# Kernel tuning notes

Hardware: AMD Instinct MI355X
Metric: run time of the kernel (lower is better)

## Reference

```python
import jax, jax.numpy as jnp
import numpy as np

B, DIN, H, DOUT, NB = 1024, 512, 1024, 512, 10
ALPHA = 0.5
INNER = 5


def setup_inputs() -> dict:
    key = jax.random.key(0)
    ks = jax.random.split(key, 5)
    return {
        "x": jax.random.normal(ks[0], (B, DIN), jnp.float32),
        "embed_W": jax.random.normal(ks[1], (H, DIN), jnp.float32) / np.float32(np.sqrt(DIN)),
        "embed_b": jnp.zeros((H,), jnp.float32),
        "block_W": jax.random.normal(ks[2], (NB, H, H), jnp.float32) * np.float32(0.8 / np.sqrt(H)),
        "block_b": jnp.zeros((NB, H), jnp.float32),
        "head_W": jax.random.normal(ks[3], (DOUT, H), jnp.float32) / np.float32(np.sqrt(H)),
        "head_b": jnp.zeros((DOUT,), jnp.float32),
        "steps": 30,
    }


def reference(x, embed_W, embed_b, block_W, block_b, head_W, head_b, steps):
    nb = block_W.shape[0]
    x_emb = x @ embed_W.T + embed_b  # [B, H]
    bb = block_b[:, None, :]  # [NB, 1, H]

    def inner_core(inp):
        # inp: [NB, B, H]; run inner equilibrium loop from h=0
        def body(h, _):
            pre = jnp.einsum('nbh,ndh->nbd', h, block_W) + bb + inp
            h = (1.0 - ALPHA) * h + ALPHA * jnp.tanh(pre)
            return h, None
        h, _ = jax.lax.scan(body, jnp.zeros_like(inp), None, length=INNER)
        return h

    def outer_step(h, _):
        # block i's input is previous-step state of block i-1 (block 0 gets x_emb)
        block_in = jnp.concatenate([x_emb[None], h[:-1]], axis=0)  # [NB, B, H]
        inner_eq = inner_core(h + block_in)
        h_new = (1.0 - ALPHA) * h + ALPHA * inner_eq
        return h_new, None

    h0 = jnp.zeros((nb,) + x_emb.shape, x_emb.dtype)
    h_final, _ = jax.lax.scan(outer_step, h0, None, length=steps)
    return h_final[-1] @ head_W.T + head_b  # [B, DOUT]
```

## Files before the change

kernel.cpp:

```cpp
#include <hip/hip_runtime.h>
#include <cstdint>
#include <cstddef>

#define B_DIM  1024
#define DIN    512
#define H_DIM  1024
#define DOUT   512
#define NB     10
#define STEPS  30

typedef _Float16 half_t;
typedef __attribute__((ext_vector_type(8))) _Float16 frag_ab;
typedef __attribute__((ext_vector_type(8))) _Float16 h8vec;
typedef __attribute__((ext_vector_type(4))) float    frag_cd;

__device__ __forceinline__ void gload16(const void* g, void* l) {
    __builtin_amdgcn_global_load_lds(
        (const __attribute__((address_space(1))) void*)g,
        (__attribute__((address_space(3))) void*)l, 16, 0, 0);
}

__device__ __forceinline__ float fast_tanh(float x) {
    float e, r;
    asm("v_exp_f32 %0, %1" : "=v"(e) : "v"(x * 2.8853900817779268f));
    asm("v_rcp_f32 %0, %1" : "=v"(r) : "v"(e + 1.0f));
    return __builtin_fmaf(-2.0f, r, 1.0f);
}

__global__ void __launch_bounds__(256)
f2h_kernel(const float* __restrict__ src, half_t* __restrict__ dst, int n4)
{
    const int i = blockIdx.x * 256 + threadIdx.x;
    if (i < n4) {
        const float4 v = ((const float4*)src)[i];
        half_t o[4] = { (half_t)v.x, (half_t)v.y, (half_t)v.z, (half_t)v.w };
        ((uint2*)dst)[i] = *(const uint2*)o;
    }
}

template <int MODE>
__global__ void __launch_bounds__(256, 2)
gemm_bt(const half_t* __restrict__ A,
        const half_t* __restrict__ W,
        const float* __restrict__ bias,
        const half_t* __restrict__ binp,
        const half_t* aux16,
        float* __restrict__ out32,
        half_t* out16,
        int M, int N, int K)
{
    const int gx  = gridDim.x, gy = gridDim.y;
    const int nwg = gx * gy * gridDim.z;
    const int f   = blockIdx.x + gx * (blockIdx.y + gy * blockIdx.z);
    const int w   = (f & 7) * (nwg >> 3) + (f >> 3);
    const int bx  = w % gx;
    const int rst = w / gx;
    const int by  = rst % gy;
    const int n   = rst / gy;

    A    += (size_t)n * M * K;
    W    += (size_t)n * N * K;
    bias += (size_t)n * N;
    if (MODE != 0) {
        const size_t so = (size_t)n * M * N;
        binp  += so;
        out16 += so;
        if (MODE == 2) aux16 += so;
    }

    const int tileM = by * 128;
    const int tileN = bx * 128;

    __shared__ __attribute__((aligned(16))) char lds_raw[65536];
    half_t* lA  = (half_t*)lds_raw;
    half_t* lB  = (half_t*)(lds_raw + 32768);
    float*  fsm = (float*)lds_raw;

    const int tid  = threadIdx.x;
    const int wave = tid >> 6;
    const int lane = tid & 63;
    const int q    = lane >> 4;
    const int r16  = lane & 15;
    const int wm   = wave >> 1;
    const int wn   = wave & 1;

    const int srow = lane >> 3;
    const int scol = ((lane & 7) ^ srow) * 8;

    const half_t* gA = A + (size_t)(tileM + wave * 32 + srow) * K + scol;
    const half_t* gW = W + (size_t)(tileN + wave * 32 + srow) * K + scol;

    auto stage = [&](int k0, int b) {
#pragma unroll
        for (int i = 0; i < 4; ++i)
            gload16(gA + (size_t)i * 8 * K + k0,
                    (void*)&lA[b * 8192 + (wave * 32 + i * 8) * 64]);
#pragma unroll
        for (int i = 0; i < 4; ++i)
            gload16(gW + (size_t)i * 8 * K + k0,
                    (void*)&lB[b * 8192 + (wave * 32 + i * 8) * 64]);
    };

    frag_cd acc[4][4];
#pragma unroll
    for (int mt = 0; mt < 4; ++mt)
#pragma unroll
        for (int nt = 0; nt < 4; ++nt)
            acc[mt][nt] = (frag_cd){0.f, 0.f, 0.f, 0.f};

    const int NT = K >> 6;
    stage(0, 0);

    int cur = 0;
    for (int t = 0; t < NT; ++t) {
        if (t + 1 < NT) {
            stage((t + 1) << 6, cur ^ 1);
            asm volatile("s_waitcnt vmcnt(8)" ::: "memory");
        } else {
            asm volatile("s_waitcnt vmcnt(0)" ::: "memory");
        }
        __builtin_amdgcn_s_barrier();
        asm volatile("" ::: "memory");

        frag_ab av[2][4], bv[2][4];
#pragma unroll
        for (int kk = 0; kk < 2; ++kk) {
            const int cb = ((kk * 4 + q) ^ (r16 & 7)) * 8;
#pragma unroll
            for (int mt = 0; mt < 4; ++mt)
                av[kk][mt] = *(const frag_ab*)&lA[cur * 8192 + (wm * 64 + mt * 16 + r16) * 64 + cb];
#pragma unroll
            for (int nt = 0; nt < 4; ++nt)
                bv[kk][nt] = *(const frag_ab*)&lB[cur * 8192 + (wn * 64 + nt * 16 + r16) * 64 + cb];
        }
#pragma unroll
        for (int kk = 0; kk < 2; ++kk)
#pragma unroll
            for (int mt = 0; mt < 4; ++mt)
#pragma unroll
                for (int nt = 0; nt < 4; ++nt)
                    acc[mt][nt] = __builtin_amdgcn_mfma_f32_16x16x32_f16(
                        av[kk][mt], bv[kk][nt], acc[mt][nt], 0, 0, 0);

        asm volatile("" ::: "memory");
        __builtin_amdgcn_s_barrier();
        cur ^= 1;
    }

    if (MODE == 0) {
#pragma unroll
        for (int mt = 0; mt < 4; ++mt)
#pragma unroll
            for (int nt = 0; nt < 4; ++nt)
#pragma unroll
                for (int r = 0; r < 4; ++r) {
                    const int row = tileM + wm * 64 + mt * 16 + q * 4 + r;
                    const int col = tileN + wn * 64 + nt * 16 + r16;
                    out32[(size_t)row * N + col] = acc[mt][nt][r] + bias[col];
                }
        return;
    }

#pragma unroll
    for (int mt = 0; mt < 4; ++mt)
#pragma unroll
        for (int nt = 0; nt < 4; ++nt)
#pragma unroll
            for (int r = 0; r < 4; ++r)
                fsm[(wm * 64 + mt * 16 + q * 4 + r) * 128 + wn * 64 + nt * 16 + r16]
                    = acc[mt][nt][r];
    __syncthreads();

#pragma unroll
    for (int c = 0; c < 8; ++c) {
        const int e   = (c * 256 + tid) * 8;
        const int rl  = e >> 7;
        const int cl  = e & 127;
        const int row = tileM + rl;
        const int col = tileN + cl;
        const size_t g = (size_t)row * N + col;

        const h8vec bi8 = *(const h8vec*)&binp[g];
        h8vec ho8, ax8;
        if (MODE == 1 || MODE == 2) ho8 = *(const h8vec*)&A[(size_t)row * K + col];
        if (MODE == 2)              ax8 = *(const h8vec*)&aux16[g];

        half_t o[8];
#pragma unroll
        for (int j = 0; j < 8; ++j) {
            const float v  = fsm[rl * 128 + cl + j];
            const float bi = (float)bi8[j];
            const float tt = fast_tanh(v + bi);
            const float ho = (MODE == 3) ? 0.5f * fast_tanh(bi) : (float)ho8[j];
            const float hn = 0.5f * ho + 0.5f * tt;
            const float ov = (MODE == 2) ? 0.5f * (float)ax8[j] + 0.5f * hn : hn;
            o[j] = (half_t)ov;
        }
        *(uint4*)&out16[g] = *(const uint4*)o;
    }
}

__global__ void __launch_bounds__(256)
pre_outer_kernel(const half_t* __restrict__ h,
                 const float* __restrict__ x_emb,
                 const float* __restrict__ bb,
                 half_t* __restrict__ binp,
                 half_t* __restrict__ hhh)
{
    const int f  = blockIdx.x;
    const int k  = f & 7;
    const int j  = f >> 3;
    const int p  = 10 * k + (j % 10);
    const int bi = j / 10;
    const int n  = p >> 3;

    const size_t idx = ((size_t)p << 17) + (size_t)bi * 2048 + (size_t)threadIdx.x * 8;
    const size_t off = idx - (size_t)n * B_DIM * H_DIM;
    const int    col = (int)(off & (H_DIM - 1));

    const h8vec ha = *(const h8vec*)&h[idx];
    float pv[8];
    if (n == 0) {
        const float4 p0 = *(const float4*)&x_emb[off];
        const float4 p1 = *(const float4*)&x_emb[off + 4];
        pv[0] = p0.x; pv[1] = p0.y; pv[2] = p0.z; pv[3] = p0.w;
        pv[4] = p1.x; pv[5] = p1.y; pv[6] = p1.z; pv[7] = p1.w;
    } else {
        const h8vec pa = *(const h8vec*)&h[idx - (size_t)B_DIM * H_DIM];
#pragma unroll
        for (int j2 = 0; j2 < 8; ++j2) pv[j2] = (float)pa[j2];
    }
    const float4 b0 = *(const float4*)&bb[(size_t)n * H_DIM + col];
    const float4 b1 = *(const float4*)&bb[(size_t)n * H_DIM + col + 4];
    const float bp[8] = {b0.x, b0.y, b0.z, b0.w, b1.x, b1.y, b1.z, b1.w};

    half_t bv[8], hv[8];
#pragma unroll
    for (int j2 = 0; j2 < 8; ++j2) {
        const float biv = (float)ha[j2] + pv[j2] + bp[j2];
        bv[j2] = (half_t)biv;
        hv[j2] = (half_t)(0.5f * fast_tanh(biv));
    }
    *(uint4*)&binp[idx] = *(const uint4*)bv;
    *(uint4*)&hhh[idx]  = *(const uint4*)hv;
}

static inline void conv(const float* src, half_t* dst, int n, hipStream_t s) {
    const int n4 = n / 4;
    f2h_kernel<<<(n4 + 255) / 256, 256, 0, s>>>(src, dst, n4);
}

extern "C" void kernel_launch(void* const* d_in, const int* in_sizes, int n_in,
                              void* d_out, int out_size, void* d_ws, size_t ws_size,
                              hipStream_t stream)
{
    const float* x     = (const float*)d_in[0];
    const float* embW  = (const float*)d_in[1];
    const float* embB  = (const float*)d_in[2];
    const float* blkW  = (const float*)d_in[3];
    const float* blkB  = (const float*)d_in[4];
    const float* headW = (const float*)d_in[5];
    const float* headB = (const float*)d_in[6];
    float* out = (float*)d_out;

    char* ws = (char*)d_ws;
    size_t off = 0;
    auto alloc = [&](size_t bytes) {
        void* p = ws + off;
        off += (bytes + 255) & ~(size_t)255;
        return p;
    };
    const size_t NE = (size_t)NB * B_DIM * H_DIM;

    float* xemb32 = (float*)alloc((size_t)B_DIM * H_DIM * 4);
    half_t* h16    = (half_t*)alloc(NE * 2);
    half_t* binp16 = (half_t*)alloc(NE * 2);
    half_t* hhh0   = (half_t*)alloc(NE * 2);
    half_t* hhh1   = (half_t*)alloc(NE * 2);
    half_t* wx     = (half_t*)alloc((size_t)B_DIM * DIN * 2);
    half_t* wembW  = (half_t*)alloc((size_t)H_DIM * DIN * 2);
    half_t* wblkW  = (half_t*)alloc((size_t)NB * H_DIM * H_DIM * 2);
    half_t* wheadW = (half_t*)alloc((size_t)DOUT * H_DIM * 2);
    (void)ws_size;

    conv(x,     wx,     B_DIM * DIN,        stream);
    conv(embW,  wembW,  H_DIM * DIN,        stream);
    conv(blkW,  wblkW,  NB * H_DIM * H_DIM, stream);
    conv(headW, wheadW, DOUT * H_DIM,       stream);

    hipMemsetAsync(h16, 0, NE * 2, stream);

    const dim3 blk(256);

    gemm_bt<0><<<dim3(H_DIM / 128, B_DIM / 128, 1), blk, 0, stream>>>(
        wx, wembW, embB, nullptr, nullptr, xemb32, nullptr, B_DIM, H_DIM, DIN);

    const dim3 ggrid(H_DIM / 128, B_DIM / 128, NB);
    const int pre_blocks = (int)(NE / (8 * 256));
    for (int s = 0; s < STEPS; ++s) {
        pre_outer_kernel<<<pre_blocks, blk, 0, stream>>>(h16, xemb32, blkB, binp16, hhh0);
        gemm_bt<3><<<ggrid, blk, 0, stream>>>(hhh0, wblkW, blkB, binp16, nullptr,
                                              nullptr, hhh1, B_DIM, H_DIM, H_DIM);
        gemm_bt<1><<<ggrid, blk, 0, stream>>>(hhh1, wblkW, blkB, binp16, nullptr,
                                              nullptr, hhh0, B_DIM, H_DIM, H_DIM);
        gemm_bt<1><<<ggrid, blk, 0, stream>>>(hhh0, wblkW, blkB, binp16, nullptr,
                                              nullptr, hhh1, B_DIM, H_DIM, H_DIM);
        gemm_bt<2><<<ggrid, blk, 0, stream>>>(hhh1, wblkW, blkB, binp16, h16,
                                              nullptr, h16, B_DIM, H_DIM, H_DIM);
    }

    gemm_bt<0><<<dim3(DOUT / 128, B_DIM / 128, 1), blk, 0, stream>>>(
        h16 + (size_t)(NB - 1) * B_DIM * H_DIM, wheadW, headB, nullptr, nullptr,
        out, nullptr, B_DIM, DOUT, H_DIM);
}
```

Before: 4.594 ms.

## Halve GEMM K-tile and LDS footprint to fit four workgroups per CU

```diff
diff --git a/kernel.cpp b/kernel.cpp
--- a/kernel.cpp
+++ b/kernel.cpp
@@ -39,7 +39,7 @@
 }
 
 template <int MODE>
-__global__ void __launch_bounds__(256, 2)
+__global__ void __launch_bounds__(256, 4)
 gemm_bt(const half_t* __restrict__ A,
         const half_t* __restrict__ W,
         const float* __restrict__ bias,
@@ -71,9 +71,9 @@
     const int tileM = by * 128;
     const int tileN = bx * 128;
 
-    __shared__ __attribute__((aligned(16))) char lds_raw[65536];
+    __shared__ __attribute__((aligned(16))) char lds_raw[32768];
     half_t* lA  = (half_t*)lds_raw;
-    half_t* lB  = (half_t*)(lds_raw + 32768);
+    half_t* lB  = (half_t*)(lds_raw + 16384);
     float*  fsm = (float*)lds_raw;
 
     const int tid  = threadIdx.x;
@@ -84,21 +84,20 @@
     const int wm   = wave >> 1;
     const int wn   = wave & 1;
 
-    const int srow = lane >> 3;
-    const int scol = ((lane & 7) ^ srow) * 8;
+    const int srow = lane >> 2;
+    const int scol = ((lane & 3) ^ ((srow >> 1) & 3)) * 8;
 
     const half_t* gA = A + (size_t)(tileM + wave * 32 + srow) * K + scol;
     const half_t* gW = W + (size_t)(tileN + wave * 32 + srow) * K + scol;
 
     auto stage = [&](int k0, int b) {
 #pragma unroll
-        for (int i = 0; i < 4; ++i)
-            gload16(gA + (size_t)i * 8 * K + k0,
-                    (void*)&lA[b * 8192 + (wave * 32 + i * 8) * 64]);
-#pragma unroll
-        for (int i = 0; i < 4; ++i)
-            gload16(gW + (size_t)i * 8 * K + k0,
-                    (void*)&lB[b * 8192 + (wave * 32 + i * 8) * 64]);
+        for (int i = 0; i < 2; ++i) {
+            gload16(gA + (size_t)i * 16 * K + k0,
+                    (void*)&lA[b * 4096 + (wave * 32 + i * 16) * 32]);
+            gload16(gW + (size_t)i * 16 * K + k0,
+                    (void*)&lB[b * 4096 + (wave * 32 + i * 16) * 32]);
+        }
     };
 
     frag_cd acc[4][4];
@@ -108,39 +107,35 @@
         for (int nt = 0; nt < 4; ++nt)
             acc[mt][nt] = (frag_cd){0.f, 0.f, 0.f, 0.f};
 
-    const int NT = K >> 6;
+    const int NT = K >> 5;
     stage(0, 0);
+
+    const int cb = (q ^ ((r16 >> 1) & 3)) * 8;
 
     int cur = 0;
     for (int t = 0; t < NT; ++t) {
         if (t + 1 < NT) {
-            stage((t + 1) << 6, cur ^ 1);
-            asm volatile("s_waitcnt vmcnt(8)" ::: "memory");
+            stage((t + 1) << 5, cur ^ 1);
+            asm volatile("s_waitcnt vmcnt(4)" ::: "memory");
         } else {
             asm volatile("s_waitcnt vmcnt(0)" ::: "memory");
         }
         __builtin_amdgcn_s_barrier();
         asm volatile("" ::: "memory");
 
-        frag_ab av[2][4], bv[2][4];
-#pragma unroll
-        for (int kk = 0; kk < 2; ++kk) {
-            const int cb = ((kk * 4 + q) ^ (r16 & 7)) * 8;
-#pragma unroll
-            for (int mt = 0; mt < 4; ++mt)
-                av[kk][mt] = *(const frag_ab*)&lA[cur * 8192 + (wm * 64 + mt * 16 + r16) * 64 + cb];
+        frag_ab av[4], bv[4];
+#pragma unroll
+        for (int mt = 0; mt < 4; ++mt)
+            av[mt] = *(const frag_ab*)&lA[cur * 4096 + (wm * 64 + mt * 16 + r16) * 32 + cb];
+#pragma unroll
+        for (int nt = 0; nt < 4; ++nt)
+            bv[nt] = *(const frag_ab*)&lB[cur * 4096 + (wn * 64 + nt * 16 + r16) * 32 + cb];
+#pragma unroll
+        for (int mt = 0; mt < 4; ++mt)
 #pragma unroll
             for (int nt = 0; nt < 4; ++nt)
-                bv[kk][nt] = *(const frag_ab*)&lB[cur * 8192 + (wn * 64 + nt * 16 + r16) * 64 + cb];
-        }
-#pragma unroll
-        for (int kk = 0; kk < 2; ++kk)
-#pragma unroll
-            for (int mt = 0; mt < 4; ++mt)
-#pragma unroll
-                for (int nt = 0; nt < 4; ++nt)
-                    acc[mt][nt] = __builtin_amdgcn_mfma_f32_16x16x32_f16(
-                        av[kk][mt], bv[kk][nt], acc[mt][nt], 0, 0, 0);
+                acc[mt][nt] = __builtin_amdgcn_mfma_f32_16x16x32_f16(
+                    av[mt], bv[nt], acc[mt][nt], 0, 0, 0);
 
         asm volatile("" ::: "memory");
         __builtin_amdgcn_s_barrier();
@@ -161,42 +156,58 @@
         return;
     }
 
-#pragma unroll
-    for (int mt = 0; mt < 4; ++mt)
-#pragma unroll
-        for (int nt = 0; nt < 4; ++nt)
-#pragma unroll
-            for (int r = 0; r < 4; ++r)
-                fsm[(wm * 64 + mt * 16 + q * 4 + r) * 128 + wn * 64 + nt * 16 + r16]
-                    = acc[mt][nt][r];
-    __syncthreads();
-
-#pragma unroll
-    for (int c = 0; c < 8; ++c) {
-        const int e   = (c * 256 + tid) * 8;
-        const int rl  = e >> 7;
-        const int cl  = e & 127;
-        const int row = tileM + rl;
-        const int col = tileN + cl;
-        const size_t g = (size_t)row * N + col;
-
-        const h8vec bi8 = *(const h8vec*)&binp[g];
-        h8vec ho8, ax8;
-        if (MODE == 1 || MODE == 2) ho8 = *(const h8vec*)&A[(size_t)row * K + col];
-        if (MODE == 2)              ax8 = *(const h8vec*)&aux16[g];
-
-        half_t o[8];
-#pragma unroll
-        for (int j = 0; j < 8; ++j) {
-            const float v  = fsm[rl * 128 + cl + j];
-            const float bi = (float)bi8[j];
-            const float tt = fast_tanh(v + bi);
-            const float ho = (MODE == 3) ? 0.5f * fast_tanh(bi) : (float)ho8[j];
-            const float hn = 0.5f * ho + 0.5f * tt;
-            const float ov = (MODE == 2) ? 0.5f * (float)ax8[j] + 0.5f * hn : hn;
-            o[j] = (half_t)ov;
+    for (int pass = 0; pass < 2; ++pass) {
+        __syncthreads();
+        if (wm == pass) {
+#pragma unroll
+            for (int mt = 0; mt < 4; ++mt)
+#pragma unroll
+                for (int nt = 0; nt < 4; ++nt)
+#pragma unroll
+                    for (int r = 0; r < 4; ++r) {
+                        const int rowl = mt * 16 + q * 4 + r;
+                        const int col  = wn * 64 + nt * 16 + r16;
+                        const int g    = col >> 2;
+                        const int gl   = (g & 24) | ((g ^ (g >> 3) ^ (rowl & 7)) & 7);
+                        fsm[rowl * 128 + gl * 4 + (col & 3)] = acc[mt][nt][r];
+                    }
         }
-        *(uint4*)&out16[g] = *(const uint4*)o;
+        __syncthreads();
+
+#pragma unroll
+        for (int c = 0; c < 4; ++c) {
+            const int e    = (c * 256 + tid) * 8;
+            const int rowl = e >> 7;
+            const int col0 = e & 127;
+            const int row  = tileM + pass * 64 + rowl;
+            const int col  = tileN + col0;
+            const size_t gidx = (size_t)row * N + col;
+
+            const int g0  = col0 >> 2;
+            const int gl0 = (g0 & 24) | ((g0 ^ (g0 >> 3) ^ (rowl & 7)) & 7);
+            const int g1  = g0 + 1;
+            const int gl1 = (g1 & 24) | ((g1 ^ (g1 >> 3) ^ (rowl & 7)) & 7);
+            const float4 va = *(const float4*)&fsm[rowl * 128 + gl0 * 4];
+            const float4 vb = *(const float4*)&fsm[rowl * 128 + gl1 * 4];
+            const float vv[8] = {va.x, va.y, va.z, va.w, vb.x, vb.y, vb.z, vb.w};
+
+            const h8vec bi8 = *(const h8vec*)&binp[gidx];
+            h8vec ho8, ax8;
+            if (MODE == 1 || MODE == 2) ho8 = *(const h8vec*)&A[(size_t)row * K + col];
+            if (MODE == 2)              ax8 = *(const h8vec*)&aux16[gidx];
+
+            half_t o[8];
+#pragma unroll
+            for (int j = 0; j < 8; ++j) {
+                const float bi = (float)bi8[j];
+                const float tt = fast_tanh(vv[j] + bi);
+                const float ho = (MODE == 3) ? 0.5f * fast_tanh(bi) : (float)ho8[j];
+                const float hn = 0.5f * ho + 0.5f * tt;
+                const float ov = (MODE == 2) ? 0.5f * (float)ax8[j] + 0.5f * hn : hn;
+                o[j] = (half_t)ov;
+            }
+            *(uint4*)&out16[gidx] = *(const uint4*)o;
+        }
     }
 }
 
```

Result: slower. 6.757 ms (+47.1%).

## Use persistent 512-block grid with per-XCD tile assignment and swizzled epilogue LDS

Applied to the files above, without the earlier changes.

```diff
diff --git a/kernel.cpp b/kernel.cpp
--- a/kernel.cpp
+++ b/kernel.cpp
@@ -49,28 +49,6 @@
         half_t* out16,
         int M, int N, int K)
 {
-    const int gx  = gridDim.x, gy = gridDim.y;
-    const int nwg = gx * gy * gridDim.z;
-    const int f   = blockIdx.x + gx * (blockIdx.y + gy * blockIdx.z);
-    const int w   = (f & 7) * (nwg >> 3) + (f >> 3);
-    const int bx  = w % gx;
-    const int rst = w / gx;
-    const int by  = rst % gy;
-    const int n   = rst / gy;
-
-    A    += (size_t)n * M * K;
-    W    += (size_t)n * N * K;
-    bias += (size_t)n * N;
-    if (MODE != 0) {
-        const size_t so = (size_t)n * M * N;
-        binp  += so;
-        out16 += so;
-        if (MODE == 2) aux16 += so;
-    }
-
-    const int tileM = by * 128;
-    const int tileN = bx * 128;
-
     __shared__ __attribute__((aligned(16))) char lds_raw[65536];
     half_t* lA  = (half_t*)lds_raw;
     half_t* lB  = (half_t*)(lds_raw + 32768);
@@ -87,116 +65,165 @@
     const int srow = lane >> 3;
     const int scol = ((lane & 7) ^ srow) * 8;
 
-    const half_t* gA = A + (size_t)(tileM + wave * 32 + srow) * K + scol;
-    const half_t* gW = W + (size_t)(tileN + wave * 32 + srow) * K + scol;
-
-    auto stage = [&](int k0, int b) {
-#pragma unroll
-        for (int i = 0; i < 4; ++i)
-            gload16(gA + (size_t)i * 8 * K + k0,
-                    (void*)&lA[b * 8192 + (wave * 32 + i * 8) * 64]);
-#pragma unroll
-        for (int i = 0; i < 4; ++i)
-            gload16(gW + (size_t)i * 8 * K + k0,
-                    (void*)&lB[b * 8192 + (wave * 32 + i * 8) * 64]);
+    auto do_tile = [&](int bx, int by, int n) {
+        const half_t* An = A + (size_t)n * M * K;
+        const half_t* Wn = W + (size_t)n * N * K;
+        const float*  bn = bias + (size_t)n * N;
+        const half_t* binpn = binp;
+        const half_t* auxn  = aux16;
+        half_t* outn = out16;
+        if (MODE != 0) {
+            const size_t so = (size_t)n * M * N;
+            binpn = binp + so;
+            outn  = out16 + so;
+            if (MODE == 2) auxn = aux16 + so;
+        }
+        const int tileM = by * 128;
+        const int tileN = bx * 128;
+
+        const half_t* gA = An + (size_t)(tileM + wave * 32 + srow) * K + scol;
+        const half_t* gW = Wn + (size_t)(tileN + wave * 32 + srow) * K + scol;
+
+        auto stage = [&](int k0, int b) {
+#pragma unroll
+            for (int i = 0; i < 4; ++i)
+                gload16(gA + (size_t)i * 8 * K + k0,
+                        (void*)&lA[b * 8192 + (wave * 32 + i * 8) * 64]);
+#pragma unroll
+            for (int i = 0; i < 4; ++i)
+                gload16(gW + (size_t)i * 8 * K + k0,
+                        (void*)&lB[b * 8192 + (wave * 32 + i * 8) * 64]);
+        };
+
+        frag_cd acc[4][4];
+#pragma unroll
+        for (int mt = 0; mt < 4; ++mt)
+#pragma unroll
+            for (int nt = 0; nt < 4; ++nt)
+                acc[mt][nt] = (frag_cd){0.f, 0.f, 0.f, 0.f};
+
+        __syncthreads();
+        const int NT = K >> 6;
+        stage(0, 0);
+
+        int cur = 0;
+        for (int t = 0; t < NT; ++t) {
+            if (t + 1 < NT) {
+                stage((t + 1) << 6, cur ^ 1);
+                asm volatile("s_waitcnt vmcnt(8)" ::: "memory");
+            } else {
+                asm volatile("s_waitcnt vmcnt(0)" ::: "memory");
+            }
+            __builtin_amdgcn_s_barrier();
+            asm volatile("" ::: "memory");
+
+            frag_ab av[2][4], bv[2][4];
+#pragma unroll
+            for (int kk = 0; kk < 2; ++kk) {
+                const int cb = ((kk * 4 + q) ^ (r16 & 7)) * 8;
+#pragma unroll
+                for (int mt = 0; mt < 4; ++mt)
+                    av[kk][mt] = *(const frag_ab*)&lA[cur * 8192 + (wm * 64 + mt * 16 + r16) * 64 + cb];
+#pragma unroll
+                for (int nt = 0; nt < 4; ++nt)
+                    bv[kk][nt] = *(const frag_ab*)&lB[cur * 8192 + (wn * 64 + nt * 16 + r16) * 64 + cb];
+            }
+#pragma unroll
+            for (int kk = 0; kk < 2; ++kk)
+#pragma unroll
+                for (int mt = 0; mt < 4; ++mt)
+#pragma unroll
+                    for (int nt = 0; nt < 4; ++nt)
+                        acc[mt][nt] = __builtin_amdgcn_mfma_f32_16x16x32_f16(
+                            av[kk][mt], bv[kk][nt], acc[mt][nt], 0, 0, 0);
+
+            asm volatile("" ::: "memory");
+            __builtin_amdgcn_s_barrier();
+            cur ^= 1;
+        }
+
+        if (MODE == 0) {
+#pragma unroll
+            for (int mt = 0; mt < 4; ++mt)
+#pragma unroll
+                for (int nt = 0; nt < 4; ++nt)
+#pragma unroll
+                    for (int r = 0; r < 4; ++r) {
+                        const int row = tileM + wm * 64 + mt * 16 + q * 4 + r;
+                        const int col = tileN + wn * 64 + nt * 16 + r16;
+                        out32[(size_t)row * N + col] = acc[mt][nt][r] + bn[col];
+                    }
+            return;
+        }
+
+#pragma unroll
+        for (int mt = 0; mt < 4; ++mt)
+#pragma unroll
+            for (int nt = 0; nt < 4; ++nt)
+#pragma unroll
+                for (int r = 0; r < 4; ++r) {
+                    const int row = wm * 64 + mt * 16 + q * 4 + r;
+                    const int col = wn * 64 + nt * 16 + r16;
+                    const int g   = col >> 2;
+                    const int gl  = (g & 24) | ((g ^ (g >> 3) ^ (row & 7)) & 7);
+                    fsm[row * 128 + gl * 4 + (col & 3)] = acc[mt][nt][r];
+                }
+        __syncthreads();
+
+#pragma unroll
+        for (int c = 0; c < 8; ++c) {
+            const int e   = (c * 256 + tid) * 8;
+            const int rl  = e >> 7;
+            const int cl  = e & 127;
+            const int row = tileM + rl;
+            const int col = tileN + cl;
+            const size_t gidx = (size_t)row * N + col;
+
+            const int g0  = cl >> 2;
+            const int gl0 = (g0 & 24) | ((g0 ^ (g0 >> 3) ^ (rl & 7)) & 7);
+            const int g1  = g0 + 1;
+            const int gl1 = (g1 & 24) | ((g1 ^ (g1 >> 3) ^ (rl & 7)) & 7);
+            const float4 va = *(const float4*)&fsm[rl * 128 + gl0 * 4];
+            const float4 vb = *(const float4*)&fsm[rl * 128 + gl1 * 4];
+            const float vv[8] = {va.x, va.y, va.z, va.w, vb.x, vb.y, vb.z, vb.w};
+
+            const h8vec bi8 = *(const h8vec*)&binpn[gidx];
+            h8vec ho8, ax8;
+            if (MODE == 1 || MODE == 2) ho8 = *(const h8vec*)&An[(size_t)row * K + col];
+            if (MODE == 2)              ax8 = *(const h8vec*)&auxn[gidx];
+
+            half_t o[8];
+#pragma unroll
+            for (int j = 0; j < 8; ++j) {
+                const float bi = (float)bi8[j];
+                const float tt = fast_tanh(vv[j] + bi);
+                const float ho = (MODE == 3) ? 0.5f * fast_tanh(bi) : (float)ho8[j];
+                const float hn = 0.5f * ho + 0.5f * tt;
+                const float ov = (MODE == 2) ? 0.5f * (float)ax8[j] + 0.5f * hn : hn;
+                o[j] = (half_t)ov;
+            }
+            *(uint4*)&outn[gidx] = *(const uint4*)o;
+        }
     };
 
-    frag_cd acc[4][4];
-#pragma unroll
-    for (int mt = 0; mt < 4; ++mt)
-#pragma unroll
-        for (int nt = 0; nt < 4; ++nt)
-            acc[mt][nt] = (frag_cd){0.f, 0.f, 0.f, 0.f};
-
-    const int NT = K >> 6;
-    stage(0, 0);
-
-    int cur = 0;
-    for (int t = 0; t < NT; ++t) {
-        if (t + 1 < NT) {
-            stage((t + 1) << 6, cur ^ 1);
-            asm volatile("s_waitcnt vmcnt(8)" ::: "memory");
-        } else {
-            asm volatile("s_waitcnt vmcnt(0)" ::: "memory");
-        }
-        __builtin_amdgcn_s_barrier();
-        asm volatile("" ::: "memory");
-
-        frag_ab av[2][4], bv[2][4];
-#pragma unroll
-        for (int kk = 0; kk < 2; ++kk) {
-            const int cb = ((kk * 4 + q) ^ (r16 & 7)) * 8;
-#pragma unroll
-            for (int mt = 0; mt < 4; ++mt)
-                av[kk][mt] = *(const frag_ab*)&lA[cur * 8192 + (wm * 64 + mt * 16 + r16) * 64 + cb];
-#pragma unroll
-            for (int nt = 0; nt < 4; ++nt)
-                bv[kk][nt] = *(const frag_ab*)&lB[cur * 8192 + (wn * 64 + nt * 16 + r16) * 64 + cb];
-        }
-#pragma unroll
-        for (int kk = 0; kk < 2; ++kk)
-#pragma unroll
-            for (int mt = 0; mt < 4; ++mt)
-#pragma unroll
-                for (int nt = 0; nt < 4; ++nt)
-                    acc[mt][nt] = __builtin_amdgcn_mfma_f32_16x16x32_f16(
-                        av[kk][mt], bv[kk][nt], acc[mt][nt], 0, 0, 0);
-
-        asm volatile("" ::: "memory");
-        __builtin_amdgcn_s_barrier();
-        cur ^= 1;
-    }
-
     if (MODE == 0) {
-#pragma unroll
-        for (int mt = 0; mt < 4; ++mt)
-#pragma unroll
-            for (int nt = 0; nt < 4; ++nt)
-#pragma unroll
-                for (int r = 0; r < 4; ++r) {
-                    const int row = tileM + wm * 64 + mt * 16 + q * 4 + r;
-                    const int col = tileN + wn * 64 + nt * 16 + r16;
-                    out32[(size_t)row * N + col] = acc[mt][nt][r] + bias[col];
-                }
-        return;
-    }
-
-#pragma unroll
-    for (int mt = 0; mt < 4; ++mt)
-#pragma unroll
-        for (int nt = 0; nt < 4; ++nt)
-#pragma unroll
-            for (int r = 0; r < 4; ++r)
-                fsm[(wm * 64 + mt * 16 + q * 4 + r) * 128 + wn * 64 + nt * 16 + r16]
-                    = acc[mt][nt][r];
-    __syncthreads();
-
-#pragma unroll
-    for (int c = 0; c < 8; ++c) {
-        const int e   = (c * 256 + tid) * 8;
-        const int rl  = e >> 7;
-        const int cl  = e & 127;
-        const int row = tileM + rl;
-        const int col = tileN + cl;
-        const size_t g = (size_t)row * N + col;
-
-        const h8vec bi8 = *(const h8vec*)&binp[g];
-        h8vec ho8, ax8;
-        if (MODE == 1 || MODE == 2) ho8 = *(const h8vec*)&A[(size_t)row * K + col];
-        if (MODE == 2)              ax8 = *(const h8vec*)&aux16[g];
-
-        half_t o[8];
-#pragma unroll
-        for (int j = 0; j < 8; ++j) {
-            const float v  = fsm[rl * 128 + cl + j];
-            const float bi = (float)bi8[j];
-            const float tt = fast_tanh(v + bi);
-            const float ho = (MODE == 3) ? 0.5f * fast_tanh(bi) : (float)ho8[j];
-            const float hn = 0.5f * ho + 0.5f * tt;
-            const float ov = (MODE == 2) ? 0.5f * (float)ax8[j] + 0.5f * hn : hn;
-            o[j] = (half_t)ov;
-        }
-        *(uint4*)&out16[g] = *(const uint4*)o;
+        const int gx  = gridDim.x, gy = gridDim.y;
+        const int nwg = gx * gy * gridDim.z;
+        const int f   = blockIdx.x + gx * (blockIdx.y + gy * blockIdx.z);
+        const int w   = (f & 7) * (nwg >> 3) + (f >> 3);
+        const int bx  = w % gx;
+        const int rst = w / gx;
+        do_tile(bx, rst % gy, rst / gy);
+    } else {
+        const int f   = blockIdx.x;
+        const int xcd = f & 7;
+        const int j   = f >> 3;
+        const int w1  = xcd * 80 + j;
+        do_tile(w1 & 7, (w1 >> 3) & 7, w1 >> 6);
+        if (j < 16) {
+            const int w2 = xcd * 80 + 64 + j;
+            do_tile(w2 & 7, (w2 >> 3) & 7, w2 >> 6);
+        }
     }
 }
 
@@ -295,7 +322,7 @@
     gemm_bt<0><<<dim3(H_DIM / 128, B_DIM / 128, 1), blk, 0, stream>>>(
         wx, wembW, embB, nullptr, nullptr, xemb32, nullptr, B_DIM, H_DIM, DIN);
 
-    const dim3 ggrid(H_DIM / 128, B_DIM / 128, NB);
+    const int ggrid = 512;
     const int pre_blocks = (int)(NE / (8 * 256));
     for (int s = 0; s < STEPS; ++s) {
         pre_outer_kernel<<<pre_blocks, blk, 0, stream>>>(h16, xemb32, blkB, binp16, hhh0);
```

After: 4.697 ms. 2.2% more time.
